# Performance work log

Measured on AMD Instinct MI355X. Metric: run time of the kernel, lower is better.

## Reference

```python
import math
import jax, jax.numpy as jnp
import numpy as np

N_LAYERS = 30
RC = 64        # residual_channels
N_MELS = 80
TED = 128      # time_emb_dim
CD = 256       # text_dim
B, T = 8, 8192
EPS = 1e-12    # F.normalize eps


def conv1d(x, w, b, dilation=1, padding=0):
    # x: [B,C,T], w: [O,I,K], b: [O]
    y = jax.lax.conv_general_dilated(
        x, w, window_strides=(1,), padding=[(padding, padding)],
        rhs_dilation=(dilation,), dimension_numbers=("NCH", "OIH", "NCH"))
    return y + b[None, :, None]


def sinusoidal_embedding(t, dim):
    half = dim // 2
    freqs = jnp.exp(jnp.arange(half, dtype=jnp.float32) * (-math.log(10000.0) / (half - 1)))
    ang = t.astype(jnp.float32)[:, None] * freqs[None, :]
    return jnp.concatenate([jnp.sin(ang), jnp.cos(ang)], axis=1)  # [B, dim]


def mish(x):
    return x * jnp.tanh(jax.nn.softplus(x))


def setup_inputs() -> dict:
    key = jax.random.key(0)
    ks = jax.random.split(key, 24)
    s = 0.05
    inp = {
        "x": jax.random.normal(ks[0], (B, 1, N_MELS, T), jnp.float32),
        "t": jax.random.randint(ks[1], (B,), 0, 1000),
        "c_emb": jax.random.normal(ks[2], (B, CD), jnp.float32),
        # input_proj: Conv1d(n_mels, RC, 1)
        "in_w": jax.random.normal(ks[3], (RC, N_MELS, 1), jnp.float32) * s,
        "in_b": jnp.zeros((RC,), jnp.float32),
        # time MLP: Linear(TED, 4*TED), Mish, Linear(4*TED, TED). torch weight [out,in]
        "te_w1": jax.random.normal(ks[4], (4 * TED, TED), jnp.float32) * s,
        "te_b1": jnp.zeros((4 * TED,), jnp.float32),
        "te_w2": jax.random.normal(ks[5], (TED, 4 * TED), jnp.float32) * s,
        "te_b2": jnp.zeros((TED,), jnp.float32),
        # per-layer stacked params
        "dconv_w": jax.random.normal(ks[6], (N_LAYERS, 2 * RC, RC, 3), jnp.float32) * s,
        "dconv_b": jnp.zeros((N_LAYERS, 2 * RC), jnp.float32),
        "tproj_w": jax.random.normal(ks[7], (N_LAYERS, 2 * RC, TED), jnp.float32) * s,
        "tproj_b": jnp.zeros((N_LAYERS, 2 * RC), jnp.float32),
        "cproj_w": jax.random.normal(ks[8], (N_LAYERS, 2 * RC, CD), jnp.float32) * s,
        "cproj_b": jnp.zeros((N_LAYERS, 2 * RC), jnp.float32),
        "rs_w": jax.random.normal(ks[9], (N_LAYERS, 2 * RC, RC, 1), jnp.float32) * s,
        "rs_b": jnp.zeros((N_LAYERS, 2 * RC), jnp.float32),
        "skip_w": jax.random.normal(ks[10], (RC, RC, 1), jnp.float32) * s,
        "skip_b": jnp.zeros((RC,), jnp.float32),
        "out_w": jax.random.normal(ks[11], (N_MELS, RC, 1), jnp.float32) * s,
        "out_b": jnp.zeros((N_MELS,), jnp.float32),
    }
    return inp


def reference(x, t, c_emb, in_w, in_b, te_w1, te_b1, te_w2, te_b2,
              dconv_w, dconv_b, tproj_w, tproj_b, cproj_w, cproj_b,
              rs_w, rs_b, skip_w, skip_b, out_w, out_b):
    h = x[:, 0]                                  # squeeze(1) -> [B, n_mels, T]
    h = conv1d(h, in_w, in_b)                    # [B, RC, T]
    te = sinusoidal_embedding(t, TED)
    te = mish(te @ te_w1.T + te_b1) @ te_w2.T + te_b2   # [B, TED]

    skips = jnp.zeros_like(conv1d(h, rs_w[0], rs_b[0])[:, :RC])  # [B, RC, T]
    skips = jnp.zeros((h.shape[0], RC, h.shape[2]), h.dtype)
    for i in range(N_LAYERS):
        dil = 2 ** (i % 10)
        g = conv1d(h, dconv_w[i], dconv_b[i], dilation=dil, padding=dil)  # [B, 2RC, T]
        tp = (te @ tproj_w[i].T + tproj_b[i])[:, :, None]                 # [B, 2RC, 1]
        tp = tp / jnp.maximum(jnp.abs(tp), EPS)      # F.normalize over size-1 dim
        cp = (c_emb @ cproj_w[i].T + cproj_b[i])[:, :, None]
        cp = cp / jnp.maximum(jnp.abs(cp), EPS)
        g = g + tp + cp
        gate, filt = g[:, :RC], g[:, RC:]            # chunk(2, dim=1)
        out = jnp.tanh(filt) * jax.nn.sigmoid(gate)
        rs = conv1d(out, rs_w[i], rs_b[i])           # [B, 2RC, T]
        res, skip = rs[:, :RC], rs[:, RC:]
        h = h + res * (1.0 / math.sqrt(2.0))
        skips = skips + skip

    y = skips / math.sqrt(N_LAYERS)
    y = jax.nn.relu(conv1d(y, skip_w, skip_b))
    y = conv1d(y, out_w, out_b)                      # [B, n_mels, T]
    return y[:, None]                                # unsqueeze(1)
```

## Files before the change

kernel.cpp:

```cpp
#include <hip/hip_runtime.h>
#include <hip/hip_bf16.h>
#include <math.h>

#define NL 30
#define NM 80
#define Bx 8
#define Tx 8192

typedef short short8 __attribute__((ext_vector_type(8)));
typedef float f32x4 __attribute__((ext_vector_type(4)));
typedef unsigned int u32x2 __attribute__((ext_vector_type(2)));
typedef unsigned int u32x4 __attribute__((ext_vector_type(4)));

__device__ __forceinline__ float bf2f(unsigned short u) {
    union { unsigned int u; float f; } v; v.u = ((unsigned int)u) << 16; return v.f;
}
__device__ __forceinline__ unsigned short f2bf(float f) {
    union { float f; unsigned int u; } v; v.f = f;
    unsigned int r = v.u + 0x7FFFu + ((v.u >> 16) & 1u);
    return (unsigned short)(r >> 16);
}

#if defined(__has_builtin)
#if __has_builtin(__builtin_amdgcn_global_load_lds)
#define HAS_GLL 1
#endif
#endif

__device__ __forceinline__ void gll16(const void* g, void* l) {
#ifdef HAS_GLL
    __builtin_amdgcn_global_load_lds(
        (const __attribute__((address_space(1))) void*)g,
        (__attribute__((address_space(3))) void*)l, 16, 0, 0);
#else
    int lane = threadIdx.x & 63;
    *(u32x4*)((char*)l + lane * 16) = *(const u32x4*)((const char*)g + lane * 16);
#endif
}

__global__ void te_kernel(const int* __restrict__ tin,
                          const float* __restrict__ w1, const float* __restrict__ b1,
                          const float* __restrict__ w2, const float* __restrict__ b2,
                          float* __restrict__ te_out) {
    __shared__ float emb[128];
    __shared__ float h1s[512];
    __shared__ float red[512];
    int b = blockIdx.x, tid = threadIdx.x;
    if (tid < 64) {
        float fr = expf(-(float)tid * (logf(10000.f) / 63.f));
        float ang = (float)tin[b] * fr;
        emb[tid] = sinf(ang);
        emb[tid + 64] = cosf(ang);
    }
    __syncthreads();
    float a = b1[tid];
    const float* wr = w1 + tid * 128;
    for (int k = 0; k < 128; ++k) a = fmaf(emb[k], wr[k], a);
    float sp = (a > 15.f) ? a : log1pf(expf(a));
    h1s[tid] = a * tanhf(sp);
    __syncthreads();
    int o = tid & 127, q = tid >> 7;
    float p = 0.f;
    const float* wr2 = w2 + o * 512 + q * 128;
    const float* hq = h1s + q * 128;
    for (int k = 0; k < 128; ++k) p = fmaf(hq[k], wr2[k], p);
    red[tid] = p;
    __syncthreads();
    if (q == 0)
        te_out[b * 128 + o] = b2[o] + red[o] + red[o + 128] + red[o + 256] + red[o + 384];
}

__global__ void gbias_kernel(const float* __restrict__ te,
                             const float* __restrict__ cemb,
                             const float* __restrict__ tpw, const float* __restrict__ tpb,
                             const float* __restrict__ cpw, const float* __restrict__ cpb,
                             const float* __restrict__ dcb,
                             float* __restrict__ gbias) {
    int l = blockIdx.x >> 3;
    int b = blockIdx.x & 7;
    int tid = threadIdx.x, wid = tid >> 6, lane = tid & 63;
    float te0 = te[b * 128 + lane];
    float te1 = te[b * 128 + 64 + lane];
    float ce0 = cemb[b * 256 + lane];
    float ce1 = cemb[b * 256 + 64 + lane];
    float ce2 = cemb[b * 256 + 128 + lane];
    float ce3 = cemb[b * 256 + 192 + lane];
    #pragma unroll 4
    for (int i = 0; i < 16; ++i) {
        int ch = i * 8 + wid;
        const float* wr = tpw + (size_t)(l * 128 + ch) * 128;
        float s = te0 * wr[lane] + te1 * wr[lane + 64];
        const float* wc = cpw + (size_t)(l * 128 + ch) * 256;
        float sc = ce0 * wc[lane] + ce1 * wc[lane + 64] + ce2 * wc[lane + 128] + ce3 * wc[lane + 192];
        #pragma unroll
        for (int off = 32; off >= 1; off >>= 1) {
            s += __shfl_xor(s, off, 64);
            sc += __shfl_xor(sc, off, 64);
        }
        if (lane == 0) {
            float tp = tpb[l * 128 + ch] + s;
            float cp = cpb[l * 128 + ch] + sc;
            float s1 = tp / fmaxf(fabsf(tp), 1e-12f);
            float s2 = cp / fmaxf(fabsf(cp), 1e-12f);
            gbias[(l * 8 + b) * 128 + ch] = dcb[l * 128 + ch] + s1 + s2;
        }
    }
}

__global__ void prep_kernel(const float* __restrict__ dconv_w, const float* __restrict__ rs_w,
                            const float* __restrict__ skip_w, const float* __restrict__ out_w,
                            unsigned short* __restrict__ wc2, unsigned short* __restrict__ wr2,
                            unsigned short* __restrict__ skw16, unsigned short* __restrict__ oww16) {
    int idx = blockIdx.x * 256 + threadIdx.x;
    const int totC = NL * 24576;
    const int totR = NL * 128 * 64;
    if (idx < totC) {
        int l = idx / 24576;
        int r = idx - l * 24576;
        int c = r >> 3;
        int e = r & 7;
        int row = c >> 3;
        int p = c & 7;
        int col16 = p ^ (row & 7);
        int ic = col16 * 8 + e;
        int tap = row >> 7;
        int oc = row & 127;
        wc2[idx] = f2bf(dconv_w[((size_t)(l * 128 + oc) * 64 + ic) * 3 + tap]);
    } else if (idx < totC + totR) {
        int j = idx - totC;
        int l = j / 8192;
        int r = j - l * 8192;
        int c = r >> 3;
        int e = r & 7;
        int row = c >> 3;
        int p = c & 7;
        int col16 = p ^ (row & 7);
        int ic = col16 * 8 + e;
        wr2[j] = f2bf(rs_w[(size_t)(l * 128 + row) * 64 + ic]);
    } else if (idx < totC + totR + 4096) {
        int j = idx - totC - totR;
        skw16[j] = f2bf(skip_w[j] * 0.18257418583505536f);
    } else if (idx < totC + totR + 4096 + 5120) {
        int j = idx - totC - totR - 4096;
        oww16[j] = f2bf(out_w[j]);
    }
}

__global__ void in_conv_kernel(const float* __restrict__ x, const float* __restrict__ w,
                               const float* __restrict__ bias, unsigned short* __restrict__ h0) {
    __shared__ float wT[NM][64];
    int tid = threadIdx.x;
    for (int i = tid; i < NM * 64; i += 256) {
        int m = i >> 6, c = i & 63;
        wT[m][c] = w[c * NM + m];
    }
    __syncthreads();
    int b = blockIdx.y;
    int t = blockIdx.x * 128 + (tid >> 1);
    int ch0 = (tid & 1) * 32;
    const float* xp = x + (size_t)b * NM * Tx + t;
    float acc[32];
    #pragma unroll
    for (int c = 0; c < 32; ++c) acc[c] = bias[ch0 + c];
    for (int m = 0; m < NM; ++m) {
        float xv = xp[(size_t)m * Tx];
        #pragma unroll
        for (int c = 0; c < 32; ++c) acc[c] = fmaf(xv, wT[m][ch0 + c], acc[c]);
    }
    unsigned short* hp = h0 + ((size_t)b * Tx + t) * 64 + ch0;
    #pragma unroll
    for (int c = 0; c < 32; c += 2) {
        unsigned int p = (unsigned int)f2bf(acc[c]) | ((unsigned int)f2bf(acc[c + 1]) << 16);
        *(unsigned int*)(hp + c) = p;
    }
}

__launch_bounds__(512, 4)
__global__ void layer_kernel(const unsigned short* __restrict__ h_in,
                             unsigned short* __restrict__ h_out,
                             float* __restrict__ skips,
                             const unsigned short* __restrict__ wc2,
                             const unsigned short* __restrict__ wr2,
                             const float* __restrict__ gbias,
                             const float* __restrict__ rsb,
                             int dil, int first) {
    __shared__ __align__(16) unsigned char lds[81920];
    unsigned char* ldsA = lds;
    unsigned char* ldsR = lds + 49152;
    unsigned char* ldsO = lds + 65536;

    int tid = threadIdx.x;
    int wid = tid >> 6, lane = tid & 63, lr = lane & 15, lq = lane >> 4;

    #pragma unroll
    for (int j = 0; j < 6; ++j) {
        int cbase = j * 512 + wid * 64;
        gll16(wc2 + (size_t)(cbase + lane) * 8, ldsA + cbase * 16);
    }
    #pragma unroll
    for (int j = 0; j < 2; ++j) {
        int cbase = j * 512 + wid * 64;
        gll16(wr2 + (size_t)(cbase + lane) * 8, ldsR + cbase * 16);
    }

    int bid = blockIdx.x;
    int wg = (bid & 7) * 64 + (bid >> 3);
    int b = wg >> 6;
    int t0 = ((wg & 63) << 7) + wid * 16;

    const unsigned short* hb = h_in + (size_t)b * Tx * 64;
    short8 bv[3][2];
    #pragma unroll
    for (int tap = 0; tap < 3; ++tap) {
        int toff = (tap - 1) * dil;
        int t = t0 + lr + toff;
        bool v = ((unsigned)t < (unsigned)Tx);
        #pragma unroll
        for (int kc = 0; kc < 2; ++kc) {
            short8 z = {0, 0, 0, 0, 0, 0, 0, 0};
            if (v) z = *(const short8*)(hb + t * 64 + kc * 32 + lq * 8);
            bv[tap][kc] = z;
        }
    }

    f32x4 acc[8];
    #pragma unroll
    for (int mf = 0; mf < 8; ++mf)
        acc[mf] = *(const f32x4*)(gbias + b * 128 + mf * 16 + lq * 4);
    __syncthreads();

    #pragma unroll
    for (int tap = 0; tap < 3; ++tap) {
        #pragma unroll
        for (int kc = 0; kc < 2; ++kc) {
            #pragma unroll
            for (int mf = 0; mf < 8; ++mf) {
                int row = tap * 128 + mf * 16 + lr;
                short8 af = *(const short8*)(ldsA + row * 128 + ((kc * 64 + lq * 16) ^ ((lr & 7) << 4)));
                acc[mf] = __builtin_amdgcn_mfma_f32_16x16x32_bf16(af, bv[tap][kc], acc[mf], 0, 0, 0);
            }
        }
    }

    unsigned char* myO = ldsO + wid * 2048;
    #pragma unroll
    for (int mf = 0; mf < 4; ++mf) {
        int p = lr;
        unsigned short ob[4];
        #pragma unroll
        for (int r = 0; r < 4; ++r) {
            float g = acc[mf][r];
            float f = acc[mf + 4][r];
            f = fminf(f, 15.f);
            g = fminf(g, 30.f);
            float ea = __builtin_amdgcn_exp2f(f * 2.8853900817779268f);
            float eb = __builtin_amdgcn_exp2f(g * 1.4426950408889634f);
            float num = (ea - 1.f) * eb;
            float den = (ea + 1.f) * (1.f + eb);
            ob[r] = f2bf(num * __builtin_amdgcn_rcpf(den));
        }
        u32x2 pk;
        pk[0] = (unsigned int)ob[0] | ((unsigned int)ob[1] << 16);
        pk[1] = (unsigned int)ob[2] | ((unsigned int)ob[3] << 16);
        *(u32x2*)(myO + p * 128 + ((mf * 32 + lq * 8) ^ ((p & 7) << 4))) = pk;
    }

    int te_ = t0 + lr;
    size_t base = ((size_t)b * Tx + te_) * 64;
    u32x2 hold[4];
    f32x4 skold[4];
    #pragma unroll
    for (int mf = 0; mf < 4; ++mf) {
        hold[mf] = *(const u32x2*)(h_in + base + mf * 16 + lq * 4);
        if (!first) skold[mf] = *(const f32x4*)(skips + base + mf * 16 + lq * 4);
        else { skold[mf][0] = 0.f; skold[mf][1] = 0.f; skold[mf][2] = 0.f; skold[mf][3] = 0.f; }
    }

    f32x4 racc[8];
    #pragma unroll
    for (int mf = 0; mf < 8; ++mf)
        racc[mf] = *(const f32x4*)(rsb + mf * 16 + lq * 4);
    #pragma unroll
    for (int kc = 0; kc < 2; ++kc) {
        int p = lr;
        short8 ov = *(const short8*)(myO + p * 128 + ((kc * 64 + lq * 16) ^ ((p & 7) << 4)));
        #pragma unroll
        for (int mf = 0; mf < 8; ++mf) {
            int row = mf * 16 + lr;
            short8 af = *(const short8*)(ldsR + row * 128 + ((kc * 64 + lq * 16) ^ ((lr & 7) << 4)));
            racc[mf] = __builtin_amdgcn_mfma_f32_16x16x32_bf16(af, ov, racc[mf], 0, 0, 0);
        }
    }

    const float inv_s2 = 0.70710678118654752f;
    #pragma unroll
    for (int mf = 0; mf < 4; ++mf) {
        unsigned short* hp = (unsigned short*)&hold[mf];
        unsigned short hnew[4];
        #pragma unroll
        for (int r = 0; r < 4; ++r)
            hnew[r] = f2bf(bf2f(hp[r]) + racc[mf][r] * inv_s2);
        u32x2 hw;
        hw[0] = (unsigned int)hnew[0] | ((unsigned int)hnew[1] << 16);
        hw[1] = (unsigned int)hnew[2] | ((unsigned int)hnew[3] << 16);
        *(u32x2*)(h_out + base + mf * 16 + lq * 4) = hw;
        f32x4 sk = skold[mf] + racc[mf + 4];
        *(f32x4*)(skips + base + mf * 16 + lq * 4) = sk;
    }
}

__launch_bounds__(256, 2)
__global__ void out_kernel(const float* __restrict__ skips,
                           const unsigned short* __restrict__ skw,
                           const float* __restrict__ skb,
                           const unsigned short* __restrict__ oww,
                           const float* __restrict__ obias,
                           float* __restrict__ y) {
    __shared__ __align__(16) unsigned char ldsY[16384];
    int tid = threadIdx.x;
    int wid = tid >> 6;
    int lane = tid & 63;
    int lr = lane & 15;
    int lq = lane >> 4;

    int bid = blockIdx.x;
    int wg = (bid & 7) * 64 + (bid >> 3);
    int P0 = wg * 128 + wid * 32;
    int b = P0 >> 13;
    int t0 = P0 & 8191;

    short8 A1[4][2];
    #pragma unroll
    for (int mf = 0; mf < 4; ++mf)
        #pragma unroll
        for (int kc = 0; kc < 2; ++kc)
            A1[mf][kc] = *(const short8*)(skw + (mf * 16 + lr) * 64 + kc * 32 + lq * 8);

    short8 Bs[2][2];
    #pragma unroll
    for (int nf = 0; nf < 2; ++nf) {
        const float* sp = skips + ((size_t)P0 + nf * 16 + lr) * 64;
        #pragma unroll
        for (int kc = 0; kc < 2; ++kc) {
            f32x4 u = *(const f32x4*)(sp + kc * 32 + lq * 8);
            f32x4 v = *(const f32x4*)(sp + kc * 32 + lq * 8 + 4);
            short8 z;
            #pragma unroll
            for (int r = 0; r < 4; ++r) {
                z[r] = (short)f2bf(u[r]);
                z[r + 4] = (short)f2bf(v[r]);
            }
            Bs[nf][kc] = z;
        }
    }

    f32x4 acc1[4][2];
    #pragma unroll
    for (int mf = 0; mf < 4; ++mf) {
        f32x4 bb = *(const f32x4*)(skb + mf * 16 + lq * 4);
        acc1[mf][0] = bb;
        acc1[mf][1] = bb;
    }
    #pragma unroll
    for (int kc = 0; kc < 2; ++kc)
        #pragma unroll
        for (int mf = 0; mf < 4; ++mf) {
            acc1[mf][0] = __builtin_amdgcn_mfma_f32_16x16x32_bf16(A1[mf][kc], Bs[0][kc], acc1[mf][0], 0, 0, 0);
            acc1[mf][1] = __builtin_amdgcn_mfma_f32_16x16x32_bf16(A1[mf][kc], Bs[1][kc], acc1[mf][1], 0, 0, 0);
        }

    unsigned char* myY = ldsY + wid * 4096;
    #pragma unroll
    for (int mf = 0; mf < 4; ++mf)
        #pragma unroll
        for (int nf = 0; nf < 2; ++nf) {
            int p = nf * 16 + lr;
            unsigned short ob[4];
            #pragma unroll
            for (int r = 0; r < 4; ++r)
                ob[r] = f2bf(fmaxf(acc1[mf][nf][r], 0.f));
            u32x2 pk;
            pk[0] = (unsigned int)ob[0] | ((unsigned int)ob[1] << 16);
            pk[1] = (unsigned int)ob[2] | ((unsigned int)ob[3] << 16);
            *(u32x2*)(myY + p * 128 + ((mf * 32 + lq * 8) ^ ((p & 7) << 4))) = pk;
        }

    short8 B2[2][2];
    #pragma unroll
    for (int nf = 0; nf < 2; ++nf) {
        int p = nf * 16 + lr;
        #pragma unroll
        for (int kc = 0; kc < 2; ++kc)
            B2[nf][kc] = *(const short8*)(myY + p * 128 + ((kc * 64 + lq * 16) ^ ((p & 7) << 4)));
    }
    f32x4 acc2[5][2];
    #pragma unroll
    for (int mf = 0; mf < 5; ++mf) {
        f32x4 bb = *(const f32x4*)(obias + mf * 16 + lq * 4);
        acc2[mf][0] = bb;
        acc2[mf][1] = bb;
    }
    #pragma unroll
    for (int kc = 0; kc < 2; ++kc)
        #pragma unroll
        for (int mf = 0; mf < 5; ++mf) {
            short8 A2 = *(const short8*)(oww + (mf * 16 + lr) * 64 + kc * 32 + lq * 8);
            acc2[mf][0] = __builtin_amdgcn_mfma_f32_16x16x32_bf16(A2, B2[0][kc], acc2[mf][0], 0, 0, 0);
            acc2[mf][1] = __builtin_amdgcn_mfma_f32_16x16x32_bf16(A2, B2[1][kc], acc2[mf][1], 0, 0, 0);
        }

    #pragma unroll
    for (int mf = 0; mf < 5; ++mf)
        #pragma unroll
        for (int nf = 0; nf < 2; ++nf) {
            int t = t0 + nf * 16 + lr;
            #pragma unroll
            for (int r = 0; r < 4; ++r) {
                int m = mf * 16 + lq * 4 + r;
                y[((size_t)b * NM + m) * Tx + t] = acc2[mf][nf][r];
            }
        }
}

extern "C" void kernel_launch(void* const* d_in, const int* in_sizes, int n_in,
                              void* d_out, int out_size, void* d_ws, size_t ws_size,
                              hipStream_t stream) {
    const float* x       = (const float*)d_in[0];
    const int*   tin     = (const int*)d_in[1];
    const float* c_emb   = (const float*)d_in[2];
    const float* in_w    = (const float*)d_in[3];
    const float* in_b    = (const float*)d_in[4];
    const float* te_w1   = (const float*)d_in[5];
    const float* te_b1   = (const float*)d_in[6];
    const float* te_w2   = (const float*)d_in[7];
    const float* te_b2   = (const float*)d_in[8];
    const float* dconv_w = (const float*)d_in[9];
    const float* dconv_b = (const float*)d_in[10];
    const float* tproj_w = (const float*)d_in[11];
    const float* tproj_b = (const float*)d_in[12];
    const float* cproj_w = (const float*)d_in[13];
    const float* cproj_b = (const float*)d_in[14];
    const float* rs_w    = (const float*)d_in[15];
    const float* rs_b    = (const float*)d_in[16];
    const float* skip_w  = (const float*)d_in[17];
    const float* skip_b  = (const float*)d_in[18];
    const float* out_w   = (const float*)d_in[19];
    const float* out_b   = (const float*)d_in[20];

    char* ws = (char*)d_ws;
    float* te_buf         = (float*)(ws + 0);
    float* gbias          = (float*)(ws + 4096);
    unsigned short* skw16 = (unsigned short*)(ws + 126976);
    unsigned short* oww16 = (unsigned short*)(ws + 135168);
    unsigned short* wc2   = (unsigned short*)(ws + 145408);
    unsigned short* wr2   = (unsigned short*)(ws + 1619968);
    unsigned short* h0    = (unsigned short*)(ws + 2111488);
    unsigned short* h1    = (unsigned short*)(ws + 10500096);
    float* skips          = (float*)(ws + 18888704);

    te_kernel<<<8, 512, 0, stream>>>(tin, te_w1, te_b1, te_w2, te_b2, te_buf);
    gbias_kernel<<<240, 512, 0, stream>>>(te_buf, c_emb, tproj_w, tproj_b,
                                          cproj_w, cproj_b, dconv_b, gbias);
    prep_kernel<<<3876, 256, 0, stream>>>(dconv_w, rs_w, skip_w, out_w,
                                          wc2, wr2, skw16, oww16);
    in_conv_kernel<<<dim3(64, 8), 256, 0, stream>>>(x, in_w, in_b, h0);

    unsigned short* hin = h0;
    unsigned short* hout = h1;
    for (int i = 0; i < NL; ++i) {
        int dil = 1 << (i % 10);
        layer_kernel<<<512, 512, 0, stream>>>(hin, hout, skips,
                                              wc2 + (size_t)i * 24576,
                                              wr2 + (size_t)i * 8192,
                                              gbias + (size_t)i * 1024,
                                              rs_b + (size_t)i * 128,
                                              dil, i == 0 ? 1 : 0);
        unsigned short* tmp = hin; hin = hout; hout = tmp;
    }
    out_kernel<<<512, 256, 0, stream>>>(skips, skw16, skip_b, oww16, out_b,
                                        (float*)d_out);
}
```

Baseline: 558.8 us.

## Merge setup kernels, fuse output head into last layer, fold residual into accumulator

Merges the time-embedding, weight-prep and input-conv kernels into one launch. Fuses the final skip/output projection into the last residual layer so the fp32 skips tensor is not written and then reread, and that layer skips the unused residual half. In the regular layers, h_in and skips are loaded before the gating math, and both are folded into the MFMA accumulator init (h scaled by sqrt2). The aim is fewer launches and less memory traffic, at the cost of a heavier last-layer kernel and an extra rounding step on the residual path.

```diff
diff --git a/kernel.cpp b/kernel.cpp
--- a/kernel.cpp
+++ b/kernel.cpp
@@ -38,36 +38,108 @@
 #endif
 }
 
-__global__ void te_kernel(const int* __restrict__ tin,
-                          const float* __restrict__ w1, const float* __restrict__ b1,
-                          const float* __restrict__ w2, const float* __restrict__ b2,
-                          float* __restrict__ te_out) {
-    __shared__ float emb[128];
-    __shared__ float h1s[512];
-    __shared__ float red[512];
-    int b = blockIdx.x, tid = threadIdx.x;
-    if (tid < 64) {
-        float fr = expf(-(float)tid * (logf(10000.f) / 63.f));
-        float ang = (float)tin[b] * fr;
-        emb[tid] = sinf(ang);
-        emb[tid + 64] = cosf(ang);
-    }
-    __syncthreads();
-    float a = b1[tid];
-    const float* wr = w1 + tid * 128;
-    for (int k = 0; k < 128; ++k) a = fmaf(emb[k], wr[k], a);
-    float sp = (a > 15.f) ? a : log1pf(expf(a));
-    h1s[tid] = a * tanhf(sp);
-    __syncthreads();
-    int o = tid & 127, q = tid >> 7;
-    float p = 0.f;
-    const float* wr2 = w2 + o * 512 + q * 128;
-    const float* hq = h1s + q * 128;
-    for (int k = 0; k < 128; ++k) p = fmaf(hq[k], wr2[k], p);
-    red[tid] = p;
-    __syncthreads();
-    if (q == 0)
-        te_out[b * 128 + o] = b2[o] + red[o] + red[o + 128] + red[o + 256] + red[o + 384];
+__global__ __launch_bounds__(512) void setup_kernel(
+        const int* __restrict__ tin,
+        const float* __restrict__ w1, const float* __restrict__ b1,
+        const float* __restrict__ w2, const float* __restrict__ b2,
+        float* __restrict__ te_out,
+        const float* __restrict__ dconv_w, const float* __restrict__ rs_w,
+        const float* __restrict__ skip_w, const float* __restrict__ out_w,
+        unsigned short* __restrict__ wc2, unsigned short* __restrict__ wr2,
+        unsigned short* __restrict__ skw16, unsigned short* __restrict__ oww16,
+        const float* __restrict__ x, const float* __restrict__ in_w,
+        const float* __restrict__ in_b, unsigned short* __restrict__ h0) {
+    __shared__ float smem[5120];
+    int blk = blockIdx.x;
+    int tid = threadIdx.x;
+    if (blk < 8) {
+        float* emb = smem;
+        float* h1s = smem + 128;
+        float* red = smem + 640;
+        int b = blk;
+        if (tid < 64) {
+            float fr = expf(-(float)tid * (logf(10000.f) / 63.f));
+            float ang = (float)tin[b] * fr;
+            emb[tid] = sinf(ang);
+            emb[tid + 64] = cosf(ang);
+        }
+        __syncthreads();
+        float a = b1[tid];
+        const float* wr = w1 + tid * 128;
+        for (int k = 0; k < 128; ++k) a = fmaf(emb[k], wr[k], a);
+        float sp = (a > 15.f) ? a : log1pf(expf(a));
+        h1s[tid] = a * tanhf(sp);
+        __syncthreads();
+        int o = tid & 127, q = tid >> 7;
+        float p = 0.f;
+        const float* wr2 = w2 + o * 512 + q * 128;
+        const float* hq = h1s + q * 128;
+        for (int k = 0; k < 128; ++k) p = fmaf(hq[k], wr2[k], p);
+        red[tid] = p;
+        __syncthreads();
+        if (q == 0)
+            te_out[b * 128 + o] = b2[o] + red[o] + red[o + 128] + red[o + 256] + red[o + 384];
+    } else if (blk < 1946) {
+        int idx = (blk - 8) * 512 + tid;
+        const int totC = NL * 24576;
+        const int totR = NL * 128 * 64;
+        if (idx < totC) {
+            int l = idx / 24576;
+            int r = idx - l * 24576;
+            int c = r >> 3;
+            int e = r & 7;
+            int row = c >> 3;
+            int p = c & 7;
+            int col16 = p ^ (row & 7);
+            int ic = col16 * 8 + e;
+            int tap = row >> 7;
+            int oc = row & 127;
+            wc2[idx] = f2bf(dconv_w[((size_t)(l * 128 + oc) * 64 + ic) * 3 + tap]);
+        } else if (idx < totC + totR) {
+            int j = idx - totC;
+            int l = j / 8192;
+            int r = j - l * 8192;
+            int c = r >> 3;
+            int e = r & 7;
+            int row = c >> 3;
+            int p = c & 7;
+            int col16 = p ^ (row & 7);
+            int ic = col16 * 8 + e;
+            wr2[j] = f2bf(rs_w[(size_t)(l * 128 + row) * 64 + ic]);
+        } else if (idx < totC + totR + 4096) {
+            int j = idx - totC - totR;
+            skw16[j] = f2bf(skip_w[j] * 0.18257418583505536f);
+        } else if (idx < totC + totR + 4096 + 5120) {
+            int j = idx - totC - totR - 4096;
+            oww16[j] = f2bf(out_w[j]);
+        }
+    } else {
+        float (*wT)[64] = (float(*)[64])smem;
+        for (int i = tid; i < NM * 64; i += 512) {
+            int m = i >> 6, c = i & 63;
+            wT[m][c] = in_w[c * NM + m];
+        }
+        __syncthreads();
+        int j = blk - 1946;
+        int b = j >> 5;
+        int t = (j & 31) * 256 + (tid >> 1);
+        int ch0 = (tid & 1) * 32;
+        const float* xp = x + (size_t)b * NM * Tx + t;
+        float acc[32];
+        #pragma unroll
+        for (int c = 0; c < 32; ++c) acc[c] = in_b[ch0 + c];
+        for (int m = 0; m < NM; ++m) {
+            float xv = xp[(size_t)m * Tx];
+            #pragma unroll
+            for (int c = 0; c < 32; ++c) acc[c] = fmaf(xv, wT[m][ch0 + c], acc[c]);
+        }
+        unsigned short* hp = h0 + ((size_t)b * Tx + t) * 64 + ch0;
+        #pragma unroll
+        for (int c = 0; c < 32; c += 2) {
+            unsigned int p = (unsigned int)f2bf(acc[c]) | ((unsigned int)f2bf(acc[c + 1]) << 16);
+            *(unsigned int*)(hp + c) = p;
+        }
+    }
 }
 
 __global__ void gbias_kernel(const float* __restrict__ te,
@@ -107,74 +179,6 @@
     }
 }
 
-__global__ void prep_kernel(const float* __restrict__ dconv_w, const float* __restrict__ rs_w,
-                            const float* __restrict__ skip_w, const float* __restrict__ out_w,
-                            unsigned short* __restrict__ wc2, unsigned short* __restrict__ wr2,
-                            unsigned short* __restrict__ skw16, unsigned short* __restrict__ oww16) {
-    int idx = blockIdx.x * 256 + threadIdx.x;
-    const int totC = NL * 24576;
-    const int totR = NL * 128 * 64;
-    if (idx < totC) {
-        int l = idx / 24576;
-        int r = idx - l * 24576;
-        int c = r >> 3;
-        int e = r & 7;
-        int row = c >> 3;
-        int p = c & 7;
-        int col16 = p ^ (row & 7);
-        int ic = col16 * 8 + e;
-        int tap = row >> 7;
-        int oc = row & 127;
-        wc2[idx] = f2bf(dconv_w[((size_t)(l * 128 + oc) * 64 + ic) * 3 + tap]);
-    } else if (idx < totC + totR) {
-        int j = idx - totC;
-        int l = j / 8192;
-        int r = j - l * 8192;
-        int c = r >> 3;
-        int e = r & 7;
-        int row = c >> 3;
-        int p = c & 7;
-        int col16 = p ^ (row & 7);
-        int ic = col16 * 8 + e;
-        wr2[j] = f2bf(rs_w[(size_t)(l * 128 + row) * 64 + ic]);
-    } else if (idx < totC + totR + 4096) {
-        int j = idx - totC - totR;
-        skw16[j] = f2bf(skip_w[j] * 0.18257418583505536f);
-    } else if (idx < totC + totR + 4096 + 5120) {
-        int j = idx - totC - totR - 4096;
-        oww16[j] = f2bf(out_w[j]);
-    }
-}
-
-__global__ void in_conv_kernel(const float* __restrict__ x, const float* __restrict__ w,
-                               const float* __restrict__ bias, unsigned short* __restrict__ h0) {
-    __shared__ float wT[NM][64];
-    int tid = threadIdx.x;
-    for (int i = tid; i < NM * 64; i += 256) {
-        int m = i >> 6, c = i & 63;
-        wT[m][c] = w[c * NM + m];
-    }
-    __syncthreads();
-    int b = blockIdx.y;
-    int t = blockIdx.x * 128 + (tid >> 1);
-    int ch0 = (tid & 1) * 32;
-    const float* xp = x + (size_t)b * NM * Tx + t;
-    float acc[32];
-    #pragma unroll
-    for (int c = 0; c < 32; ++c) acc[c] = bias[ch0 + c];
-    for (int m = 0; m < NM; ++m) {
-        float xv = xp[(size_t)m * Tx];
-        #pragma unroll
-        for (int c = 0; c < 32; ++c) acc[c] = fmaf(xv, wT[m][ch0 + c], acc[c]);
-    }
-    unsigned short* hp = h0 + ((size_t)b * Tx + t) * 64 + ch0;
-    #pragma unroll
-    for (int c = 0; c < 32; c += 2) {
-        unsigned int p = (unsigned int)f2bf(acc[c]) | ((unsigned int)f2bf(acc[c + 1]) << 16);
-        *(unsigned int*)(hp + c) = p;
-    }
-}
-
 __launch_bounds__(512, 4)
 __global__ void layer_kernel(const unsigned short* __restrict__ h_in,
                              unsigned short* __restrict__ h_out,
@@ -242,6 +246,16 @@
         }
     }
 
+    size_t base = ((size_t)b * Tx + t0 + lr) * 64;
+    u32x2 hv[4];
+    f32x4 sko[4];
+    #pragma unroll
+    for (int mf = 0; mf < 4; ++mf) {
+        hv[mf] = *(const u32x2*)(h_in + base + mf * 16 + lq * 4);
+        if (!first) sko[mf] = *(const f32x4*)(skips + base + mf * 16 + lq * 4);
+        else { sko[mf][0] = 0.f; sko[mf][1] = 0.f; sko[mf][2] = 0.f; sko[mf][3] = 0.f; }
+    }
+
     unsigned char* myO = ldsO + wid * 2048;
     #pragma unroll
     for (int mf = 0; mf < 4; ++mf) {
@@ -265,21 +279,21 @@
         *(u32x2*)(myO + p * 128 + ((mf * 32 + lq * 8) ^ ((p & 7) << 4))) = pk;
     }
 
-    int te_ = t0 + lr;
-    size_t base = ((size_t)b * Tx + te_) * 64;
-    u32x2 hold[4];
-    f32x4 skold[4];
-    #pragma unroll
-    for (int mf = 0; mf < 4; ++mf) {
-        hold[mf] = *(const u32x2*)(h_in + base + mf * 16 + lq * 4);
-        if (!first) skold[mf] = *(const f32x4*)(skips + base + mf * 16 + lq * 4);
-        else { skold[mf][0] = 0.f; skold[mf][1] = 0.f; skold[mf][2] = 0.f; skold[mf][3] = 0.f; }
-    }
-
+    const float rt2 = 1.41421356237309505f;
     f32x4 racc[8];
     #pragma unroll
-    for (int mf = 0; mf < 8; ++mf)
-        racc[mf] = *(const f32x4*)(rsb + mf * 16 + lq * 4);
+    for (int mf = 0; mf < 4; ++mf) {
+        f32x4 rb = *(const f32x4*)(rsb + mf * 16 + lq * 4);
+        unsigned short* hp = (unsigned short*)&hv[mf];
+        f32x4 r;
+        #pragma unroll
+        for (int r_ = 0; r_ < 4; ++r_) r[r_] = fmaf(bf2f(hp[r_]), rt2, rb[r_]);
+        racc[mf] = r;
+    }
+    #pragma unroll
+    for (int mf = 0; mf < 4; ++mf)
+        racc[mf + 4] = *(const f32x4*)(rsb + 64 + mf * 16 + lq * 4) + sko[mf];
+
     #pragma unroll
     for (int kc = 0; kc < 2; ++kc) {
         int p = lr;
@@ -295,131 +309,189 @@
     const float inv_s2 = 0.70710678118654752f;
     #pragma unroll
     for (int mf = 0; mf < 4; ++mf) {
-        unsigned short* hp = (unsigned short*)&hold[mf];
         unsigned short hnew[4];
         #pragma unroll
         for (int r = 0; r < 4; ++r)
-            hnew[r] = f2bf(bf2f(hp[r]) + racc[mf][r] * inv_s2);
+            hnew[r] = f2bf(racc[mf][r] * inv_s2);
         u32x2 hw;
         hw[0] = (unsigned int)hnew[0] | ((unsigned int)hnew[1] << 16);
         hw[1] = (unsigned int)hnew[2] | ((unsigned int)hnew[3] << 16);
         *(u32x2*)(h_out + base + mf * 16 + lq * 4) = hw;
-        f32x4 sk = skold[mf] + racc[mf + 4];
-        *(f32x4*)(skips + base + mf * 16 + lq * 4) = sk;
-    }
-}
-
-__launch_bounds__(256, 2)
-__global__ void out_kernel(const float* __restrict__ skips,
-                           const unsigned short* __restrict__ skw,
-                           const float* __restrict__ skb,
-                           const unsigned short* __restrict__ oww,
-                           const float* __restrict__ obias,
-                           float* __restrict__ y) {
-    __shared__ __align__(16) unsigned char ldsY[16384];
+        *(f32x4*)(skips + base + mf * 16 + lq * 4) = racc[mf + 4];
+    }
+}
+
+__launch_bounds__(512, 2)
+__global__ void layer_last_kernel(const unsigned short* __restrict__ h_in,
+                                  const float* __restrict__ skips,
+                                  const unsigned short* __restrict__ wc2,
+                                  const unsigned short* __restrict__ wr2,
+                                  const float* __restrict__ gbias,
+                                  const float* __restrict__ rsb,
+                                  const unsigned short* __restrict__ skw,
+                                  const float* __restrict__ skb,
+                                  const unsigned short* __restrict__ oww,
+                                  const float* __restrict__ obias,
+                                  float* __restrict__ y,
+                                  int dil) {
+    __shared__ __align__(16) unsigned char lds[81920];
+    unsigned char* ldsA = lds;
+    unsigned char* ldsR = lds + 49152;
+    unsigned char* ldsO = lds + 65536;
+
     int tid = threadIdx.x;
-    int wid = tid >> 6;
-    int lane = tid & 63;
-    int lr = lane & 15;
-    int lq = lane >> 4;
+    int wid = tid >> 6, lane = tid & 63, lr = lane & 15, lq = lane >> 4;
+
+    #pragma unroll
+    for (int j = 0; j < 6; ++j) {
+        int cbase = j * 512 + wid * 64;
+        gll16(wc2 + (size_t)(cbase + lane) * 8, ldsA + cbase * 16);
+    }
+    #pragma unroll
+    for (int j = 0; j < 2; ++j) {
+        int cbase = j * 512 + wid * 64;
+        gll16(wr2 + (size_t)(cbase + lane) * 8, ldsR + cbase * 16);
+    }
 
     int bid = blockIdx.x;
     int wg = (bid & 7) * 64 + (bid >> 3);
-    int P0 = wg * 128 + wid * 32;
-    int b = P0 >> 13;
-    int t0 = P0 & 8191;
-
-    short8 A1[4][2];
+    int b = wg >> 6;
+    int t0 = ((wg & 63) << 7) + wid * 16;
+
+    const unsigned short* hb = h_in + (size_t)b * Tx * 64;
+    short8 bv[3][2];
+    #pragma unroll
+    for (int tap = 0; tap < 3; ++tap) {
+        int toff = (tap - 1) * dil;
+        int t = t0 + lr + toff;
+        bool v = ((unsigned)t < (unsigned)Tx);
+        #pragma unroll
+        for (int kc = 0; kc < 2; ++kc) {
+            short8 z = {0, 0, 0, 0, 0, 0, 0, 0};
+            if (v) z = *(const short8*)(hb + t * 64 + kc * 32 + lq * 8);
+            bv[tap][kc] = z;
+        }
+    }
+
+    f32x4 acc[8];
+    #pragma unroll
+    for (int mf = 0; mf < 8; ++mf)
+        acc[mf] = *(const f32x4*)(gbias + b * 128 + mf * 16 + lq * 4);
+    __syncthreads();
+
+    #pragma unroll
+    for (int tap = 0; tap < 3; ++tap) {
+        #pragma unroll
+        for (int kc = 0; kc < 2; ++kc) {
+            #pragma unroll
+            for (int mf = 0; mf < 8; ++mf) {
+                int row = tap * 128 + mf * 16 + lr;
+                short8 af = *(const short8*)(ldsA + row * 128 + ((kc * 64 + lq * 16) ^ ((lr & 7) << 4)));
+                acc[mf] = __builtin_amdgcn_mfma_f32_16x16x32_bf16(af, bv[tap][kc], acc[mf], 0, 0, 0);
+            }
+        }
+    }
+
+    size_t base = ((size_t)b * Tx + t0 + lr) * 64;
+    f32x4 sko[4];
     #pragma unroll
     for (int mf = 0; mf < 4; ++mf)
-        #pragma unroll
-        for (int kc = 0; kc < 2; ++kc)
-            A1[mf][kc] = *(const short8*)(skw + (mf * 16 + lr) * 64 + kc * 32 + lq * 8);
-
-    short8 Bs[2][2];
-    #pragma unroll
-    for (int nf = 0; nf < 2; ++nf) {
-        const float* sp = skips + ((size_t)P0 + nf * 16 + lr) * 64;
-        #pragma unroll
-        for (int kc = 0; kc < 2; ++kc) {
-            f32x4 u = *(const f32x4*)(sp + kc * 32 + lq * 8);
-            f32x4 v = *(const f32x4*)(sp + kc * 32 + lq * 8 + 4);
-            short8 z;
-            #pragma unroll
-            for (int r = 0; r < 4; ++r) {
-                z[r] = (short)f2bf(u[r]);
-                z[r + 4] = (short)f2bf(v[r]);
-            }
-            Bs[nf][kc] = z;
-        }
-    }
-
-    f32x4 acc1[4][2];
-    #pragma unroll
-    for (int mf = 0; mf < 4; ++mf) {
-        f32x4 bb = *(const f32x4*)(skb + mf * 16 + lq * 4);
-        acc1[mf][0] = bb;
-        acc1[mf][1] = bb;
-    }
-    #pragma unroll
-    for (int kc = 0; kc < 2; ++kc)
+        sko[mf] = *(const f32x4*)(skips + base + mf * 16 + lq * 4);
+
+    unsigned char* myO = ldsO + wid * 2048;
+    #pragma unroll
+    for (int mf = 0; mf < 4; ++mf) {
+        int p = lr;
+        unsigned short ob[4];
+        #pragma unroll
+        for (int r = 0; r < 4; ++r) {
+            float g = acc[mf][r];
+            float f = acc[mf + 4][r];
+            f = fminf(f, 15.f);
+            g = fminf(g, 30.f);
+            float ea = __builtin_amdgcn_exp2f(f * 2.8853900817779268f);
+            float eb = __builtin_amdgcn_exp2f(g * 1.4426950408889634f);
+            float num = (ea - 1.f) * eb;
+            float den = (ea + 1.f) * (1.f + eb);
+            ob[r] = f2bf(num * __builtin_amdgcn_rcpf(den));
+        }
+        u32x2 pk;
+        pk[0] = (unsigned int)ob[0] | ((unsigned int)ob[1] << 16);
+        pk[1] = (unsigned int)ob[2] | ((unsigned int)ob[3] << 16);
+        *(u32x2*)(myO + p * 128 + ((mf * 32 + lq * 8) ^ ((p & 7) << 4))) = pk;
+    }
+
+    f32x4 racc[4];
+    #pragma unroll
+    for (int mf = 0; mf < 4; ++mf)
+        racc[mf] = *(const f32x4*)(rsb + 64 + mf * 16 + lq * 4) + sko[mf];
+    #pragma unroll
+    for (int kc = 0; kc < 2; ++kc) {
+        int p = lr;
+        short8 ov = *(const short8*)(myO + p * 128 + ((kc * 64 + lq * 16) ^ ((p & 7) << 4)));
         #pragma unroll
         for (int mf = 0; mf < 4; ++mf) {
-            acc1[mf][0] = __builtin_amdgcn_mfma_f32_16x16x32_bf16(A1[mf][kc], Bs[0][kc], acc1[mf][0], 0, 0, 0);
-            acc1[mf][1] = __builtin_amdgcn_mfma_f32_16x16x32_bf16(A1[mf][kc], Bs[1][kc], acc1[mf][1], 0, 0, 0);
-        }
-
-    unsigned char* myY = ldsY + wid * 4096;
+            int row = 64 + mf * 16 + lr;
+            short8 af = *(const short8*)(ldsR + row * 128 + ((kc * 64 + lq * 16) ^ ((lr & 7) << 4)));
+            racc[mf] = __builtin_amdgcn_mfma_f32_16x16x32_bf16(af, ov, racc[mf], 0, 0, 0);
+        }
+    }
+
+    #pragma unroll
+    for (int mf = 0; mf < 4; ++mf) {
+        int p = lr;
+        u32x2 pk;
+        pk[0] = (unsigned int)f2bf(racc[mf][0]) | ((unsigned int)f2bf(racc[mf][1]) << 16);
+        pk[1] = (unsigned int)f2bf(racc[mf][2]) | ((unsigned int)f2bf(racc[mf][3]) << 16);
+        *(u32x2*)(myO + p * 128 + ((mf * 32 + lq * 8) ^ ((p & 7) << 4))) = pk;
+    }
+
+    f32x4 yacc[4];
     #pragma unroll
     for (int mf = 0; mf < 4; ++mf)
-        #pragma unroll
-        for (int nf = 0; nf < 2; ++nf) {
-            int p = nf * 16 + lr;
-            unsigned short ob[4];
-            #pragma unroll
-            for (int r = 0; r < 4; ++r)
-                ob[r] = f2bf(fmaxf(acc1[mf][nf][r], 0.f));
-            u32x2 pk;
-            pk[0] = (unsigned int)ob[0] | ((unsigned int)ob[1] << 16);
-            pk[1] = (unsigned int)ob[2] | ((unsigned int)ob[3] << 16);
-            *(u32x2*)(myY + p * 128 + ((mf * 32 + lq * 8) ^ ((p & 7) << 4))) = pk;
-        }
-
-    short8 B2[2][2];
-    #pragma unroll
-    for (int nf = 0; nf < 2; ++nf) {
-        int p = nf * 16 + lr;
-        #pragma unroll
-        for (int kc = 0; kc < 2; ++kc)
-            B2[nf][kc] = *(const short8*)(myY + p * 128 + ((kc * 64 + lq * 16) ^ ((p & 7) << 4)));
-    }
-    f32x4 acc2[5][2];
-    #pragma unroll
-    for (int mf = 0; mf < 5; ++mf) {
-        f32x4 bb = *(const f32x4*)(obias + mf * 16 + lq * 4);
-        acc2[mf][0] = bb;
-        acc2[mf][1] = bb;
-    }
-    #pragma unroll
-    for (int kc = 0; kc < 2; ++kc)
+        yacc[mf] = *(const f32x4*)(skb + mf * 16 + lq * 4);
+    #pragma unroll
+    for (int kc = 0; kc < 2; ++kc) {
+        int p = lr;
+        short8 Bv = *(const short8*)(myO + p * 128 + ((kc * 64 + lq * 16) ^ ((p & 7) << 4)));
+        #pragma unroll
+        for (int mf = 0; mf < 4; ++mf) {
+            short8 A1 = *(const short8*)(skw + (mf * 16 + lr) * 64 + kc * 32 + lq * 8);
+            yacc[mf] = __builtin_amdgcn_mfma_f32_16x16x32_bf16(A1, Bv, yacc[mf], 0, 0, 0);
+        }
+    }
+    #pragma unroll
+    for (int mf = 0; mf < 4; ++mf) {
+        int p = lr;
+        u32x2 pk;
+        pk[0] = (unsigned int)f2bf(fmaxf(yacc[mf][0], 0.f)) | ((unsigned int)f2bf(fmaxf(yacc[mf][1], 0.f)) << 16);
+        pk[1] = (unsigned int)f2bf(fmaxf(yacc[mf][2], 0.f)) | ((unsigned int)f2bf(fmaxf(yacc[mf][3], 0.f)) << 16);
+        *(u32x2*)(myO + p * 128 + ((mf * 32 + lq * 8) ^ ((p & 7) << 4))) = pk;
+    }
+
+    f32x4 oacc[5];
+    #pragma unroll
+    for (int mf = 0; mf < 5; ++mf)
+        oacc[mf] = *(const f32x4*)(obias + mf * 16 + lq * 4);
+    #pragma unroll
+    for (int kc = 0; kc < 2; ++kc) {
+        int p = lr;
+        short8 B2 = *(const short8*)(myO + p * 128 + ((kc * 64 + lq * 16) ^ ((p & 7) << 4)));
         #pragma unroll
         for (int mf = 0; mf < 5; ++mf) {
             short8 A2 = *(const short8*)(oww + (mf * 16 + lr) * 64 + kc * 32 + lq * 8);
-            acc2[mf][0] = __builtin_amdgcn_mfma_f32_16x16x32_bf16(A2, B2[0][kc], acc2[mf][0], 0, 0, 0);
-            acc2[mf][1] = __builtin_amdgcn_mfma_f32_16x16x32_bf16(A2, B2[1][kc], acc2[mf][1], 0, 0, 0);
-        }
-
-    #pragma unroll
-    for (int mf = 0; mf < 5; ++mf)
-        #pragma unroll
-        for (int nf = 0; nf < 2; ++nf) {
-            int t = t0 + nf * 16 + lr;
-            #pragma unroll
-            for (int r = 0; r < 4; ++r) {
-                int m = mf * 16 + lq * 4 + r;
-                y[((size_t)b * NM + m) * Tx + t] = acc2[mf][nf][r];
-            }
-        }
+            oacc[mf] = __builtin_amdgcn_mfma_f32_16x16x32_bf16(A2, B2, oacc[mf], 0, 0, 0);
+        }
+    }
+    int t = t0 + lr;
+    #pragma unroll
+    for (int mf = 0; mf < 5; ++mf) {
+        #pragma unroll
+        for (int r = 0; r < 4; ++r) {
+            int m = mf * 16 + lq * 4 + r;
+            y[((size_t)b * NM + m) * Tx + t] = oacc[mf][r];
+        }
+    }
 }
 
 extern "C" void kernel_launch(void* const* d_in, const int* in_sizes, int n_in,
@@ -458,16 +530,16 @@
     unsigned short* h1    = (unsigned short*)(ws + 10500096);
     float* skips          = (float*)(ws + 18888704);
 
-    te_kernel<<<8, 512, 0, stream>>>(tin, te_w1, te_b1, te_w2, te_b2, te_buf);
+    setup_kernel<<<2202, 512, 0, stream>>>(tin, te_w1, te_b1, te_w2, te_b2, te_buf,
+                                           dconv_w, rs_w, skip_w, out_w,
+                                           wc2, wr2, skw16, oww16,
+                                           x, in_w, in_b, h0);
     gbias_kernel<<<240, 512, 0, stream>>>(te_buf, c_emb, tproj_w, tproj_b,
                                           cproj_w, cproj_b, dconv_b, gbias);
-    prep_kernel<<<3876, 256, 0, stream>>>(dconv_w, rs_w, skip_w, out_w,
-                                          wc2, wr2, skw16, oww16);
-    in_conv_kernel<<<dim3(64, 8), 256, 0, stream>>>(x, in_w, in_b, h0);
 
     unsigned short* hin = h0;
     unsigned short* hout = h1;
-    for (int i = 0; i < NL; ++i) {
+    for (int i = 0; i < NL - 1; ++i) {
         int dil = 1 << (i % 10);
         layer_kernel<<<512, 512, 0, stream>>>(hin, hout, skips,
                                               wc2 + (size_t)i * 24576,
@@ -477,6 +549,11 @@
                                               dil, i == 0 ? 1 : 0);
         unsigned short* tmp = hin; hin = hout; hout = tmp;
     }
-    out_kernel<<<512, 256, 0, stream>>>(skips, skw16, skip_b, oww16, out_b,
-                                        (float*)d_out);
-}
+    layer_last_kernel<<<512, 512, 0, stream>>>(hin, skips,
+                                               wc2 + (size_t)(NL - 1) * 24576,
+                                               wr2 + (size_t)(NL - 1) * 8192,
+                                               gbias + (size_t)(NL - 1) * 1024,
+                                               rs_b + (size_t)(NL - 1) * 128,
+                                               skw16, skip_b, oww16, out_b,
+                                               (float*)d_out, 1 << ((NL - 1) % 10));
+}
```

Result: no change. 563.7 us (+0.9%).
